# Kernel tuning notes

Measured on AMD Instinct MI355X. Metric: run time of the kernel, lower is better.

The kernel has to match this reference:

```python
import jax, jax.numpy as jnp
import numpy as np

N = 200_000   # nodes
E = 6_400_000 # edges (avg degree 32)


def setup_inputs() -> dict:
    key = jax.random.key(0)
    k0, k1, k2, k3 = jax.random.split(key, 4)
    x = jax.random.normal(k0, (N, 2), dtype=jnp.float32)
    edge_index = jax.random.randint(k1, (2, E), 0, N, dtype=jnp.int32)
    W1 = jax.random.normal(k2, (2, 16), dtype=jnp.float32) * 0.5
    b1 = jnp.zeros((16,), dtype=jnp.float32)
    W2 = jax.random.normal(k3, (16, 2), dtype=jnp.float32) * 0.25
    b2 = jnp.zeros((2,), dtype=jnp.float32)
    return {"x": x, "edge_index": edge_index, "W1": W1, "b1": b1, "W2": W2, "b2": b2}


def _gcn_conv(x, W, b, src, dst):
    # PyG GCNConv: linear transform, add self-loops, symmetric deg^-1/2 norm,
    # scatter-add aggregation by destination, then bias.
    h = x @ W  # [N, out]
    ones = jnp.ones(src.shape[0], dtype=h.dtype)
    deg = jax.ops.segment_sum(ones, dst, num_segments=N)  # in-degree incl. self-loops
    dinv = jnp.where(deg > 0, jax.lax.rsqrt(deg), 0.0)
    norm = dinv[src] * dinv[dst]                  # [E+N]
    msg = h[src] * norm[:, None]                  # edge-wise gather + scale
    out = jax.ops.segment_sum(msg, dst, num_segments=N)
    return out + b


def reference(x, edge_index, W1, b1, W2, b2):
    loop = jnp.arange(N, dtype=edge_index.dtype)
    src = jnp.concatenate([edge_index[0], loop])  # add self-loops once
    dst = jnp.concatenate([edge_index[1], loop])
    h = jax.nn.relu(_gcn_conv(x, W1, b1, src, dst))
    # dropout is identity in eval mode (training=False)
    return _gcn_conv(h, W2, b2, src, dst)
```

## Files before the change

### kernel.cpp

```cpp
#include <hip/hip_runtime.h>


typedef unsigned int u32;

#define BUCKET_BITS 9
#define BUCKET_SIZE (1 << BUCKET_BITS)
#define MAX_NBUCK 512
#define PCHUNK 8192
#define STHREADS 512
#define MAX_NB 1024
#define LDSCAP 17408

__global__ void part_hist_kernel(const int* __restrict__ dst, u32* __restrict__ part,
                                 int E, int nbuck) {
    __shared__ u32 h[MAX_NBUCK];
    int t = threadIdx.x, c = blockIdx.x;
    h[t] = 0;
    __syncthreads();
    int start = c * PCHUNK, end = min(start + PCHUNK, E);
    for (int i = start + t; i < end; i += STHREADS)
        atomicAdd(&h[((u32)dst[i]) >> BUCKET_BITS], 1u);
    __syncthreads();
    for (int j = t; j < nbuck; j += STHREADS)
        part[(size_t)c * nbuck + j] = h[j];
}

__global__ void colscan_kernel(u32* __restrict__ part, u32* __restrict__ cnt,
                               int NB, int nbuck) {
    __shared__ u32 s[MAX_NB];
    int t = threadIdx.x, j = blockIdx.x;
    u32 v = (t < NB) ? part[(size_t)t * nbuck + j] : 0u;
    s[t] = v;
    for (int o = 1; o < MAX_NB; o <<= 1) {
        __syncthreads();
        u32 u = (t >= o) ? s[t - o] : 0u;
        __syncthreads();
        s[t] += u;
    }
    __syncthreads();
    if (t < NB) part[(size_t)t * nbuck + j] = s[t] - v;
    if (t == MAX_NB - 1) cnt[j] = s[MAX_NB - 1];
}

__global__ void offsets_kernel(const u32* __restrict__ cnt, u32* __restrict__ offsets,
                               int nbuck) {
    __shared__ u32 s[MAX_NBUCK];
    int t = threadIdx.x;
    u32 v = (t < nbuck) ? cnt[t] : 0u;
    s[t] = v;
    for (int o = 1; o < MAX_NBUCK; o <<= 1) {
        __syncthreads();
        u32 u = (t >= o) ? s[t - o] : 0u;
        __syncthreads();
        s[t] += u;
    }
    __syncthreads();
    if (t < nbuck) offsets[t + 1] = s[t];
    if (t == 0) offsets[0] = 0;
}

__global__ void __launch_bounds__(STHREADS)
scatter_kernel(const int* __restrict__ src, const int* __restrict__ dst,
               const u32* __restrict__ part, const u32* __restrict__ cnt,
               const u32* __restrict__ offsets, u32* __restrict__ sorted,
               int E, int nbuck, int NB) {
    __shared__ u32 pk[PCHUNK];
    __shared__ u32 ga[PCHUNK];
    __shared__ u32 gbase[MAX_NBUCK];
    __shared__ u32 scr[MAX_NBUCK];
    __shared__ u32 lbase[MAX_NBUCK];
    int t = threadIdx.x, c = blockIdx.x;
    int start = c * PCHUNK, end = min(start + PCHUNK, E);
    int cntE = end - start;

    u32 v;
    if (t < nbuck) {
        u32 pc = part[(size_t)c * nbuck + t];
        u32 nx = (c + 1 < NB) ? part[(size_t)(c + 1) * nbuck + t] : cnt[t];
        v = nx - pc;
        gbase[t] = offsets[t] + pc;
    } else {
        v = 0;
        gbase[t] = 0;
    }
    scr[t] = v;
    for (int o = 1; o < MAX_NBUCK; o <<= 1) {
        __syncthreads();
        u32 u = (t >= o) ? scr[t - o] : 0u;
        __syncthreads();
        scr[t] += u;
    }
    __syncthreads();
    lbase[t] = scr[t] - v;
    scr[t] = 0;
    __syncthreads();
    for (int i = start + t; i < end; i += STHREADS) {
        u32 d = (u32)dst[i];
        u32 b = d >> BUCKET_BITS;
        u32 p = lbase[b] + atomicAdd(&scr[b], 1u);
        pk[p] = ((u32)src[i] << BUCKET_BITS) | (d & (BUCKET_SIZE - 1));
        ga[p] = gbase[b] + (p - lbase[b]);
    }
    __syncthreads();
    for (int i = t; i < cntE; i += STHREADS)
        sorted[ga[i]] = pk[i];
}

__global__ void __launch_bounds__(STHREADS)
sort2_kernel(u32* __restrict__ sorted ,
             const u32* __restrict__ offsets, const float2* __restrict__ x,
             u32* __restrict__ noff, float* __restrict__ dinv,
             float2* __restrict__ y, int N) {
    __shared__ u32 buf[LDSCAP];
    __shared__ u32 cnt[BUCKET_SIZE];
    __shared__ u32 scn[BUCKET_SIZE];
    int t = threadIdx.x, b = blockIdx.x;
    u32 e0 = offsets[b];
    u32 len = offsets[b + 1] - e0;
    if (len > LDSCAP) len = LDSCAP;

    cnt[t] = 0;
    __syncthreads();
    for (u32 i = t; i < len; i += STHREADS)
        atomicAdd(&cnt[sorted[e0 + i] & (BUCKET_SIZE - 1)], 1u);
    __syncthreads();
    u32 v = cnt[t];
    scn[t] = v;
    for (int o = 1; o < BUCKET_SIZE; o <<= 1) {
        __syncthreads();
        u32 u = (t >= o) ? scn[t - o] : 0u;
        __syncthreads();
        scn[t] += u;
    }
    __syncthreads();
    u32 lb = scn[t] - v;
    int node = (b << BUCKET_BITS) + t;
    if (node < N) {
        noff[node] = e0 + lb;
        float di = rsqrtf((float)v + 1.0f);
        dinv[node] = di;
        float2 xv = x[node];
        y[node] = make_float2(di * xv.x, di * xv.y);
    }
    cnt[t] = lb;
    __syncthreads();
    for (u32 i = t; i < len; i += STHREADS) {
        u32 e = sorted[e0 + i];
        u32 p = atomicAdd(&cnt[e & (BUCKET_SIZE - 1)], 1u);
        buf[p] = e >> BUCKET_BITS;
    }
    __syncthreads();
    for (u32 i = t; i < len; i += STHREADS)
        sorted[e0 + i] = buf[i];
}

__global__ void __launch_bounds__(256)
agg1_mlp_kernel(const u32* __restrict__ ssrc, const u32* __restrict__ noff,
                const float2* __restrict__ y, const float* __restrict__ dinv,
                const float* __restrict__ W1, const float* __restrict__ b1,
                const float* __restrict__ W2,
                float2* __restrict__ gp, int N, u32 E) {
    int tid = blockIdx.x * blockDim.x + threadIdx.x;
    int node = tid >> 2, sub = tid & 3;
    if (node >= N) return;
    u32 i0 = noff[node];
    u32 e1 = (node + 1 < N) ? noff[node + 1] : E;
    u32 len = e1 - i0;
    u32 i = i0 + (len * (u32)sub) / 4;
    u32 q1 = i0 + (len * (u32)(sub + 1)) / 4;
    float sx = 0.f, sy = 0.f;
    for (; i + 4 <= q1; i += 4) {
        u32 s0 = ssrc[i], s1 = ssrc[i + 1], s2 = ssrc[i + 2], s3 = ssrc[i + 3];
        float2 v0 = y[s0], v1 = y[s1], v2 = y[s2], v3 = y[s3];
        sx += (v0.x + v1.x) + (v2.x + v3.x);
        sy += (v0.y + v1.y) + (v2.y + v3.y);
    }
    for (; i < q1; ++i) {
        float2 v = y[ssrc[i]];
        sx += v.x; sy += v.y;
    }
    sx += __shfl_xor(sx, 1); sy += __shfl_xor(sy, 1);
    sx += __shfl_xor(sx, 2); sy += __shfl_xor(sy, 2);
    if (sub == 0) {
        float2 yv = y[node];
        float di = dinv[node];
        float ax = di * (sx + yv.x), ay = di * (sy + yv.y);
        float g0 = 0.f, g1 = 0.f;
#pragma unroll
        for (int j = 0; j < 16; ++j) {
            float h = fmaf(ax, W1[j], fmaf(ay, W1[16 + j], b1[j]));
            h = fmaxf(h, 0.f);
            g0 = fmaf(h, W2[2 * j], g0);
            g1 = fmaf(h, W2[2 * j + 1], g1);
        }
        gp[node] = make_float2(di * g0, di * g1);
    }
}

__global__ void __launch_bounds__(256)
agg2_kernel(const u32* __restrict__ ssrc, const u32* __restrict__ noff,
            const float2* __restrict__ gp, const float* __restrict__ dinv,
            const float* __restrict__ b2, float2* __restrict__ out, int N, u32 E) {
    int tid = blockIdx.x * blockDim.x + threadIdx.x;
    int node = tid >> 2, sub = tid & 3;
    if (node >= N) return;
    u32 i0 = noff[node];
    u32 e1 = (node + 1 < N) ? noff[node + 1] : E;
    u32 len = e1 - i0;
    u32 i = i0 + (len * (u32)sub) / 4;
    u32 q1 = i0 + (len * (u32)(sub + 1)) / 4;
    float sx = 0.f, sy = 0.f;
    for (; i + 4 <= q1; i += 4) {
        u32 s0 = ssrc[i], s1 = ssrc[i + 1], s2 = ssrc[i + 2], s3 = ssrc[i + 3];
        float2 v0 = gp[s0], v1 = gp[s1], v2 = gp[s2], v3 = gp[s3];
        sx += (v0.x + v1.x) + (v2.x + v3.x);
        sy += (v0.y + v1.y) + (v2.y + v3.y);
    }
    for (; i < q1; ++i) {
        float2 v = gp[ssrc[i]];
        sx += v.x; sy += v.y;
    }
    sx += __shfl_xor(sx, 1); sy += __shfl_xor(sy, 1);
    sx += __shfl_xor(sx, 2); sy += __shfl_xor(sy, 2);
    if (sub == 0) {
        float2 gv = gp[node];
        float di = dinv[node];
        out[node] = make_float2(fmaf(di, sx + gv.x, b2[0]),
                                fmaf(di, sy + gv.y, b2[1]));
    }
}

extern "C" void kernel_launch(void* const* d_in, const int* in_sizes, int n_in,
                              void* d_out, int out_size, void* d_ws, size_t ws_size,
                              hipStream_t stream) {
    const float2* x  = (const float2*)d_in[0];
    const int*    ei = (const int*)d_in[1];
    const float*  W1 = (const float*)d_in[2];
    const float*  b1 = (const float*)d_in[3];
    const float*  W2 = (const float*)d_in[4];
    const float*  b2 = (const float*)d_in[5];

    const int N = in_sizes[0] / 2;
    const int E = in_sizes[1] / 2;
    const int* src = ei;
    const int* dst = ei + E;
    const int nbuck = (N + BUCKET_SIZE - 1) >> BUCKET_BITS;
    const int NB    = (E + PCHUNK - 1) / PCHUNK;

    u32* sorted   = (u32*)d_ws;
    float* dinv   = (float*)(sorted + E);
    float* y      = dinv + N;
    float* gp     = y + 2 * (size_t)N;
    u32* noff     = (u32*)(gp + 2 * (size_t)N);
    u32* cnt      = noff + N;
    u32* offsets  = cnt + MAX_NBUCK;
    u32* part     = (u32*)y;
    float2* out   = (float2*)d_out;

    part_hist_kernel<<<NB, STHREADS, 0, stream>>>(dst, part, E, nbuck);
    colscan_kernel  <<<nbuck, MAX_NB, 0, stream>>>(part, cnt, NB, nbuck);
    offsets_kernel  <<<1, MAX_NBUCK, 0, stream>>>(cnt, offsets, nbuck);
    scatter_kernel  <<<NB, STHREADS, 0, stream>>>(src, dst, part, cnt, offsets,
                                                  sorted, E, nbuck, NB);
    sort2_kernel    <<<nbuck, STHREADS, 0, stream>>>(sorted, offsets, x, noff, dinv,
                                                     (float2*)y, N);
    agg1_mlp_kernel <<<(4 * N + 255) / 256, 256, 0, stream>>>(sorted, noff,
                                                              (const float2*)y, dinv,
                                                              W1, b1, W2,
                                                              (float2*)gp, N, (u32)E);
    agg2_kernel     <<<(4 * N + 255) / 256, 256, 0, stream>>>(sorted, noff,
                                                              (const float2*)gp, dinv,
                                                              b2, out, N, (u32)E);
}
```

Baseline: 146.6 us.

## Use wave-shuffle block scans, pack scatter bookkeeping, and widen aggregation to 8 lanes per node

```diff
diff --git a/kernel.cpp b/kernel.cpp
--- a/kernel.cpp
+++ b/kernel.cpp
@@ -2,6 +2,7 @@
 
 
 typedef unsigned int u32;
+typedef unsigned short u16;
 
 #define BUCKET_BITS 9
 #define BUCKET_SIZE (1 << BUCKET_BITS)
@@ -59,51 +60,62 @@
     if (t == 0) offsets[0] = 0;
 }
 
+__device__ __forceinline__ u32 block_exscan512(u32 v, u32* wtot ) {
+    int t = threadIdx.x, lane = t & 63, wid = t >> 6;
+    u32 x = v;
+#pragma unroll
+    for (int d = 1; d < 64; d <<= 1) {
+        u32 u = __shfl_up(x, d);
+        if (lane >= d) x += u;
+    }
+    if (lane == 63) wtot[wid] = x;
+    __syncthreads();
+    u32 woff = 0;
+#pragma unroll
+    for (int w = 0; w < 8; ++w) {
+        u32 wv = wtot[w];
+        woff += (w < wid) ? wv : 0u;
+    }
+    __syncthreads();
+    return woff + x - v;
+}
+
 __global__ void __launch_bounds__(STHREADS)
 scatter_kernel(const int* __restrict__ src, const int* __restrict__ dst,
                const u32* __restrict__ part, const u32* __restrict__ cnt,
                const u32* __restrict__ offsets, u32* __restrict__ sorted,
                int E, int nbuck, int NB) {
     __shared__ u32 pk[PCHUNK];
-    __shared__ u32 ga[PCHUNK];
-    __shared__ u32 gbase[MAX_NBUCK];
+    __shared__ u16 bk[PCHUNK];
     __shared__ u32 scr[MAX_NBUCK];
-    __shared__ u32 lbase[MAX_NBUCK];
+    __shared__ u32 dadj[MAX_NBUCK];
+    __shared__ u32 wtot[8];
     int t = threadIdx.x, c = blockIdx.x;
     int start = c * PCHUNK, end = min(start + PCHUNK, E);
     int cntE = end - start;
 
-    u32 v;
+    u32 v = 0, gb = 0;
     if (t < nbuck) {
         u32 pc = part[(size_t)c * nbuck + t];
         u32 nx = (c + 1 < NB) ? part[(size_t)(c + 1) * nbuck + t] : cnt[t];
         v = nx - pc;
-        gbase[t] = offsets[t] + pc;
-    } else {
-        v = 0;
-        gbase[t] = 0;
-    }
-    scr[t] = v;
-    for (int o = 1; o < MAX_NBUCK; o <<= 1) {
-        __syncthreads();
-        u32 u = (t >= o) ? scr[t - o] : 0u;
-        __syncthreads();
-        scr[t] += u;
-    }
-    __syncthreads();
-    lbase[t] = scr[t] - v;
-    scr[t] = 0;
+        gb = offsets[t] + pc;
+    }
+    u32 lb = block_exscan512(v, wtot);
+    scr[t] = lb << 16;
+    dadj[t] = gb - lb;
     __syncthreads();
     for (int i = start + t; i < end; i += STHREADS) {
         u32 d = (u32)dst[i];
         u32 b = d >> BUCKET_BITS;
-        u32 p = lbase[b] + atomicAdd(&scr[b], 1u);
+        u32 old = atomicAdd(&scr[b], 1u);
+        u32 p = (old >> 16) + (old & 0xFFFFu);
         pk[p] = ((u32)src[i] << BUCKET_BITS) | (d & (BUCKET_SIZE - 1));
-        ga[p] = gbase[b] + (p - lbase[b]);
+        bk[p] = (u16)b;
     }
     __syncthreads();
     for (int i = t; i < cntE; i += STHREADS)
-        sorted[ga[i]] = pk[i];
+        sorted[dadj[bk[i]] + i] = pk[i];
 }
 
 __global__ void __launch_bounds__(STHREADS)
@@ -113,7 +125,7 @@
              float2* __restrict__ y, int N) {
     __shared__ u32 buf[LDSCAP];
     __shared__ u32 cnt[BUCKET_SIZE];
-    __shared__ u32 scn[BUCKET_SIZE];
+    __shared__ u32 wtot[8];
     int t = threadIdx.x, b = blockIdx.x;
     u32 e0 = offsets[b];
     u32 len = offsets[b + 1] - e0;
@@ -125,15 +137,7 @@
         atomicAdd(&cnt[sorted[e0 + i] & (BUCKET_SIZE - 1)], 1u);
     __syncthreads();
     u32 v = cnt[t];
-    scn[t] = v;
-    for (int o = 1; o < BUCKET_SIZE; o <<= 1) {
-        __syncthreads();
-        u32 u = (t >= o) ? scn[t - o] : 0u;
-        __syncthreads();
-        scn[t] += u;
-    }
-    __syncthreads();
-    u32 lb = scn[t] - v;
+    u32 lb = block_exscan512(v, wtot);
     int node = (b << BUCKET_BITS) + t;
     if (node < N) {
         noff[node] = e0 + lb;
@@ -161,13 +165,13 @@
                 const float* __restrict__ W2,
                 float2* __restrict__ gp, int N, u32 E) {
     int tid = blockIdx.x * blockDim.x + threadIdx.x;
-    int node = tid >> 2, sub = tid & 3;
+    int node = tid >> 3, sub = tid & 7;
     if (node >= N) return;
     u32 i0 = noff[node];
     u32 e1 = (node + 1 < N) ? noff[node + 1] : E;
     u32 len = e1 - i0;
-    u32 i = i0 + (len * (u32)sub) / 4;
-    u32 q1 = i0 + (len * (u32)(sub + 1)) / 4;
+    u32 i = i0 + (len * (u32)sub) / 8;
+    u32 q1 = i0 + (len * (u32)(sub + 1)) / 8;
     float sx = 0.f, sy = 0.f;
     for (; i + 4 <= q1; i += 4) {
         u32 s0 = ssrc[i], s1 = ssrc[i + 1], s2 = ssrc[i + 2], s3 = ssrc[i + 3];
@@ -181,6 +185,7 @@
     }
     sx += __shfl_xor(sx, 1); sy += __shfl_xor(sy, 1);
     sx += __shfl_xor(sx, 2); sy += __shfl_xor(sy, 2);
+    sx += __shfl_xor(sx, 4); sy += __shfl_xor(sy, 4);
     if (sub == 0) {
         float2 yv = y[node];
         float di = dinv[node];
@@ -202,13 +207,13 @@
             const float2* __restrict__ gp, const float* __restrict__ dinv,
             const float* __restrict__ b2, float2* __restrict__ out, int N, u32 E) {
     int tid = blockIdx.x * blockDim.x + threadIdx.x;
-    int node = tid >> 2, sub = tid & 3;
+    int node = tid >> 3, sub = tid & 7;
     if (node >= N) return;
     u32 i0 = noff[node];
     u32 e1 = (node + 1 < N) ? noff[node + 1] : E;
     u32 len = e1 - i0;
-    u32 i = i0 + (len * (u32)sub) / 4;
-    u32 q1 = i0 + (len * (u32)(sub + 1)) / 4;
+    u32 i = i0 + (len * (u32)sub) / 8;
+    u32 q1 = i0 + (len * (u32)(sub + 1)) / 8;
     float sx = 0.f, sy = 0.f;
     for (; i + 4 <= q1; i += 4) {
         u32 s0 = ssrc[i], s1 = ssrc[i + 1], s2 = ssrc[i + 2], s3 = ssrc[i + 3];
@@ -222,6 +227,7 @@
     }
     sx += __shfl_xor(sx, 1); sy += __shfl_xor(sy, 1);
     sx += __shfl_xor(sx, 2); sy += __shfl_xor(sy, 2);
+    sx += __shfl_xor(sx, 4); sy += __shfl_xor(sy, 4);
     if (sub == 0) {
         float2 gv = gp[node];
         float di = dinv[node];
@@ -264,11 +270,11 @@
                                                   sorted, E, nbuck, NB);
     sort2_kernel    <<<nbuck, STHREADS, 0, stream>>>(sorted, offsets, x, noff, dinv,
                                                      (float2*)y, N);
-    agg1_mlp_kernel <<<(4 * N + 255) / 256, 256, 0, stream>>>(sorted, noff,
+    agg1_mlp_kernel <<<(8 * N + 255) / 256, 256, 0, stream>>>(sorted, noff,
                                                               (const float2*)y, dinv,
                                                               W1, b1, W2,
                                                               (float2*)gp, N, (u32)E);
-    agg2_kernel     <<<(4 * N + 255) / 256, 256, 0, stream>>>(sorted, noff,
+    agg2_kernel     <<<(8 * N + 255) / 256, 256, 0, stream>>>(sorted, noff,
                                                               (const float2*)gp, dinv,
                                                               b2, out, N, (u32)E);
 }
```

Measured after the change: 142.1 us. 1.03x faster.
